# Kernel tuning notes

Hardware: AMD Instinct MI355X
Metric: run time of the kernel (lower is better)

The kernel has to match this reference:

```python
import jax, jax.numpy as jnp
import numpy as np

D_HEAD = 64
NEG_INF = jnp.float32(-jnp.inf)


def setup_inputs() -> dict:
    key = jax.random.key(0)
    ks = jax.random.split(key, 6)
    B, S, D, N, H = 8, 1024, 768, 12, 64
    init = 0.02
    return {
        "normalized_resid_pre": jax.random.normal(ks[0], (B, S, D), jnp.float32),
        "W_Q": jax.random.normal(ks[1], (N, D, H), jnp.float32) * init,
        "W_K": jax.random.normal(ks[2], (N, D, H), jnp.float32) * init,
        "W_V": jax.random.normal(ks[3], (N, D, H), jnp.float32) * init,
        "W_O": jax.random.normal(ks[4], (N, H, D), jnp.float32) * init,
        "b_Q": jnp.zeros((N, H), jnp.float32),
        "b_K": jnp.zeros((N, H), jnp.float32),
        "b_V": jnp.zeros((N, H), jnp.float32),
        "b_O": jnp.zeros((D,), jnp.float32),
    }


def _causal_mask(attn_scores):
    # Faithful to the source: keep entries where triu(scores, 1) != scores
    # (i.e. lower triangle incl. diagonal), set the rest to -inf.
    return jnp.where(jnp.triu(attn_scores, k=1) != attn_scores, attn_scores, NEG_INF)


def reference(normalized_resid_pre, W_Q, W_K, W_V, W_O, b_Q, b_K, b_V, b_O):
    x = normalized_resid_pre  # [b, p, d]
    keys = jnp.einsum('bpd,ndh->bpnh', x, W_K) + b_K
    queries = jnp.einsum('bpd,ndh->bpnh', x, W_Q) + b_Q
    attn_scores = jnp.einsum('bknh,bqnh->bnqk', keys, queries)  # [b, n, s_q, s_k]
    attn_probs = jax.nn.softmax(_causal_mask(attn_scores / np.sqrt(D_HEAD)), axis=-1)
    values = jnp.einsum('bpd,ndh->bpnh', x, W_V) + b_V
    z = jnp.einsum('bknh,bnqk->bqnh', values, attn_probs)
    attn_out = jnp.einsum('bpnh,nhe->bpe', z, W_O) + b_O
    return attn_out
```

## Files before the change

kernel.cpp:

```cpp
#include <hip/hip_runtime.h>
#include <stdint.h>

typedef __attribute__((ext_vector_type(4))) float f32x4;
typedef __attribute__((ext_vector_type(8))) __bf16 bf16v8;
typedef __attribute__((ext_vector_type(8))) unsigned short u16x8;
typedef __attribute__((ext_vector_type(4))) unsigned short u16x4;
typedef unsigned short u16;

#define AS1 __attribute__((address_space(1)))
#define AS3 __attribute__((address_space(3)))

__device__ __forceinline__ u16 f2b(float f) {
  union { __bf16 h; u16 u; } c; c.h = (__bf16)f; return c.u;
}

__device__ __forceinline__ f32x4 mfma16(bf16v8 a, bf16v8 b, f32x4 c) {
  return __builtin_amdgcn_mfma_f32_16x16x32_bf16(a, b, c, 0, 0, 0);
}

__device__ __forceinline__ void gl_lds16(const void* g, void* l) {
  __builtin_amdgcn_global_load_lds((AS1 void*)g, (AS3 void*)l, 16, 0, 0);
}

__global__ __launch_bounds__(256) void pack_x_kernel(
    const float* __restrict__ x, u16* __restrict__ xb, int n8,
    const float* __restrict__ bq, const float* __restrict__ bk,
    float* __restrict__ bc, float sq) {
  int i = blockIdx.x * 256 + threadIdx.x;
  if (i < n8) {
    const f32x4* p = (const f32x4*)(x + (size_t)i * 8);
    f32x4 a = p[0], b = p[1];
    u16x8 o;
    o[0] = f2b(a[0]); o[1] = f2b(a[1]); o[2] = f2b(a[2]); o[3] = f2b(a[3]);
    o[4] = f2b(b[0]); o[5] = f2b(b[1]); o[6] = f2b(b[2]); o[7] = f2b(b[3]);
    *(u16x8*)(xb + (size_t)i * 8) = o;
  } else {
    int j = i - n8;
    if (j < 768) bc[j] = bq[j] * sq;
    else if (j < 1536) bc[j] = bk[j - 768];
  }
}

__global__ __launch_bounds__(256) void pack_w_all(
    const float* __restrict__ wq, const float* __restrict__ wk,
    const float* __restrict__ wv, const float* __restrict__ wo,
    u16* __restrict__ btqk, u16* __restrict__ wvt, u16* __restrict__ wot,
    float sq) {
  __shared__ float t[64][65];
  const int z = blockIdx.z;
  const int which = z / 12, n = z % 12;
  const int c = threadIdx.x & 63, w = threadIdx.x >> 6;

  const float* in; u16* out; int in_rs, out_ns; float scale;
  int a0, b0;
  if (which == 0) { in = wq; out = btqk;          in_rs = 64;  out_ns = 49152; scale = sq;  }
  else if (which == 1) { in = wk; out = btqk + 589824; in_rs = 64; out_ns = 49152; scale = 1.f; }
  else if (which == 2) { in = wv; out = wvt;      in_rs = 64;  out_ns = 49152; scale = 1.f; }
  else { in = wo; out = wot;                      in_rs = 768; out_ns = 64;    scale = 1.f; }
  if (which < 3) { a0 = blockIdx.x * 64; b0 = 0; }
  else           { a0 = 0; b0 = blockIdx.x * 64; }

  const float* ip = in + (size_t)n * 49152;
#pragma unroll
  for (int i = 0; i < 16; ++i) {
    int r = i * 4 + w;
    t[r][c] = ip[(size_t)(a0 + r) * in_rs + (b0 + c)];
  }
  __syncthreads();
  u16* op = out + (size_t)n * out_ns;
#pragma unroll
  for (int i = 0; i < 16; ++i) {
    int r = i * 4 + w;
    op[(size_t)(b0 + r) * 768 + (a0 + c)] = f2b(t[c][r] * scale);
  }
}

template <int OUTF32, int BIASROW, int TN>
__global__ __launch_bounds__(256, 3) void gemm_bt(
    const u16* __restrict__ A, const u16* __restrict__ Bt,
    void* __restrict__ Cv, const float* __restrict__ bias, float scale, int N) {
  constexpr int K = 768;
  constexpr int MI = (TN == 128) ? 4 : 2;
  __shared__ u16 lA[2][128 * 32];
  __shared__ u16 lB[2][TN * 32];
  constexpr int BBUF = TN * 64;

  const int tid = threadIdx.x;
  const int lane = tid & 63, wid = tid >> 6;
  const int g = lane >> 4, l16 = lane & 15;
  const int rowb = (TN == 128) ? (wid >> 1) * 64 : wid * 32;
  const int colb = (TN == 128) ? (wid & 1) * 64 : 0;
  const int m0 = blockIdx.x * 128, n0 = blockIdx.y * TN;

  const int srow = tid >> 2;
  const int scol = (tid & 3) * 16;

  f32x4 acc[MI][4];
#pragma unroll
  for (int i = 0; i < MI; ++i)
#pragma unroll
    for (int j = 0; j < 4; ++j) acc[i][j] = (f32x4)0.f;

  const char* Ab = (const char*)(A + (size_t)m0 * K);
  const char* Bb = (const char*)(Bt + (size_t)n0 * K);
  char* lAb = (char*)&lA[0][0];
  char* lBb = (char*)&lB[0][0];

#define STAGE(buf, kt)                                                          \
  do {                                                                          \
    int kb = (kt) * 64;                                                         \
    gl_lds16(Ab + (size_t)srow * 1536 + kb + scol,                              \
             lAb + (buf) * 8192 + wid * 1024);                                  \
    gl_lds16(Ab + (size_t)(64 + srow) * 1536 + kb + scol,                       \
             lAb + (buf) * 8192 + 4096 + wid * 1024);                           \
    if (TN == 128) {                                                            \
      gl_lds16(Bb + (size_t)srow * 1536 + kb + scol,                            \
               lBb + (buf) * BBUF + wid * 1024);                                \
      gl_lds16(Bb + (size_t)(64 + srow) * 1536 + kb + scol,                     \
               lBb + (buf) * BBUF + 4096 + wid * 1024);                         \
    } else if (srow < 64) {                                                     \
      gl_lds16(Bb + (size_t)srow * 1536 + kb + scol,                            \
               lBb + (buf) * BBUF + wid * 1024);                                \
    }                                                                           \
  } while (0)

  STAGE(0, 0);
  __syncthreads();

  for (int kt = 0; kt < 24; ++kt) {
    const int cur = kt & 1;
    if (kt + 1 < 24) STAGE(cur ^ 1, kt + 1);
    bf16v8 af[MI], bfv[4];
#pragma unroll
    for (int i = 0; i < MI; ++i)
      af[i] = *(const bf16v8*)&lA[cur][(rowb + i * 16 + l16) * 32 + g * 8];
#pragma unroll
    for (int j = 0; j < 4; ++j)
      bfv[j] = *(const bf16v8*)&lB[cur][(colb + j * 16 + l16) * 32 + g * 8];
#pragma unroll
    for (int i = 0; i < MI; ++i)
#pragma unroll
      for (int j = 0; j < 4; ++j)
        acc[i][j] = mfma16(af[i], bfv[j], acc[i][j]);
    __syncthreads();
  }
#undef STAGE

  const int row0 = m0 + rowb, col0 = n0 + colb;
#pragma unroll
  for (int j = 0; j < 4; ++j) {
    const int col = col0 + j * 16 + l16;
    const float bcol = BIASROW ? 0.f : bias[col];
#pragma unroll
    for (int i = 0; i < MI; ++i) {
#pragma unroll
      for (int r = 0; r < 4; ++r) {
        const int row = row0 + i * 16 + g * 4 + r;
        const float bv = BIASROW ? bias[row] : bcol;
        const float v = (acc[i][j][r] + bv) * scale;
        if (OUTF32) ((float*)Cv)[(size_t)row * N + col] = v;
        else        ((u16*)Cv)[(size_t)row * N + col] = f2b(v);
      }
    }
  }
}

__global__ __launch_bounds__(256, 3) void flash7_kernel(
    const u16* __restrict__ QK, const u16* __restrict__ Vt,
    u16* __restrict__ Z) {
  __shared__ u16 lK[2][64 * 64];
  __shared__ u16 lV[2][64 * 64];
  __shared__ u16 lP[64 * 72];

  const int tid = threadIdx.x;
  const int lane = tid & 63, wid = tid >> 6;
  const int g = lane >> 4, l16 = lane & 15;

  const int id = blockIdx.x;
  const int xs = id & 7;
  const int rest = id >> 3;
  const int p = rest & 7;
  const int j = rest >> 3;
  const int head = xs + 8 * j;
  const int b = head / 12, n = head % 12;

  const int nchA = 16 - p;
  const int total = 17;

  const u16* Qh = QK + (size_t)b * 1024 * 1536 + n * 64;
  const u16* Kh = Qh + 768;
  const u16* Vh = Vt + (size_t)n * 64 * 8192 + b * 1024;
  u16* Zh = Z + (size_t)b * 1024 * 768 + n * 64;
  u16* myP = &lP[(wid * 16) * 72];

  const int srow8 = lane >> 3;
  const int sslot = lane & 7;
  const int scol = ((sslot ^ srow8) << 4);

#define FSTAGE(buf, c)                                                        \
  do {                                                                        \
    const int kv0_ = (c) << 6;                                                \
    const char* kb_ = (const char*)Kh + (size_t)(kv0_ + (wid << 4)) * 3072;   \
    const char* vb_ = (const char*)Vh + (size_t)(wid << 4) * 16384 +          \
                      (size_t)kv0_ * 2;                                       \
    gl_lds16(kb_ + (size_t)srow8 * 3072 + scol,                               \
             (char*)&lK[buf][0] + (wid << 11));                               \
    gl_lds16(kb_ + (size_t)(8 + srow8) * 3072 + scol,                         \
             (char*)&lK[buf][0] + (wid << 11) + 1024);                        \
    gl_lds16(vb_ + (size_t)srow8 * 16384 + scol,                              \
             (char*)&lV[buf][0] + (wid << 11));                               \
    gl_lds16(vb_ + (size_t)(8 + srow8) * 16384 + scol,                        \
             (char*)&lV[buf][0] + (wid << 11) + 1024);                        \
  } while (0)

#define SWZ(row, slot) (((row) << 6) + ((((slot) ^ ((row) & 7))) << 3))

  const int qwA = (15 - p) * 64 + wid * 16;
  const int qwB = p * 64 + wid * 16;
  bf16v8 qfA[2], qfB[2];
#pragma unroll
  for (int kk = 0; kk < 2; ++kk) {
    qfA[kk] = *(const bf16v8*)(Qh + (size_t)(qwA + l16) * 1536 + kk * 32 + g * 8);
    qfB[kk] = *(const bf16v8*)(Qh + (size_t)(qwB + l16) * 1536 + kk * 32 + g * 8);
  }

  f32x4 po[4];
#pragma unroll
  for (int ht = 0; ht < 4; ++ht) po[ht] = (f32x4)0.f;
  float m = -3e38f, l = 0.f;

  FSTAGE(0, 0);

  for (int s = 0; s < total; ++s) {
    const int cur = s & 1;
    const bool phB = s >= nchA;
    const int c = phB ? s - nchA : s;
    const int kv0 = c << 6;
    const int qw = phB ? qwB : qwA;

    if (s + 1 < total) {
      const int s1 = s + 1;
      const int c1 = (s1 >= nchA) ? s1 - nchA : s1;
      FSTAGE(cur ^ 1, c1);
      asm volatile("s_waitcnt vmcnt(4)" ::: "memory");
    } else {
      asm volatile("s_waitcnt vmcnt(0)" ::: "memory");
    }
    __builtin_amdgcn_s_barrier();
    __builtin_amdgcn_sched_barrier(0);

    const bf16v8 q0 = phB ? qfB[0] : qfA[0];
    const bf16v8 q1 = phB ? qfB[1] : qfA[1];

    bf16v8 kf[4][2];
#pragma unroll
    for (int kvt = 0; kvt < 4; ++kvt)
#pragma unroll
      for (int kk = 0; kk < 2; ++kk)
        kf[kvt][kk] =
            *(const bf16v8*)&lK[cur][SWZ(kvt * 16 + l16, kk * 4 + g)];
    f32x4 s_[4];
#pragma unroll
    for (int kvt = 0; kvt < 4; ++kvt) {
      f32x4 a = (f32x4)0.f;
      a = mfma16(kf[kvt][0], q0, a);
      a = mfma16(kf[kvt][1], q1, a);
      s_[kvt] = a;
    }
    bf16v8 vf[4][2];
#pragma unroll
    for (int ht = 0; ht < 4; ++ht)
#pragma unroll
      for (int kk = 0; kk < 2; ++kk)
        vf[ht][kk] =
            *(const bf16v8*)&lV[cur][SWZ(ht * 16 + l16, kk * 4 + g)];

    if (kv0 + 63 > qw) {
      const int qq = qw + l16;
#pragma unroll
      for (int kvt = 0; kvt < 4; ++kvt) {
        const int kv = kv0 + kvt * 16 + g * 4;
#pragma unroll
        for (int r = 0; r < 4; ++r)
          if (kv + r > qq) s_[kvt][r] = -3e38f;
      }
    }
    {
      float cm = s_[0][0];
#pragma unroll
      for (int kvt = 0; kvt < 4; ++kvt)
#pragma unroll
        for (int r = 0; r < 4; ++r) cm = fmaxf(cm, s_[kvt][r]);
      cm = fmaxf(cm, __shfl_xor(cm, 16));
      cm = fmaxf(cm, __shfl_xor(cm, 32));
      const bool defer = __all(cm - m <= 8.0f);
      float scl = 1.0f;
      if (!defer) {
        const float mn = fmaxf(m, cm);
        scl = exp2f(m - mn);
        m = mn;
#pragma unroll
        for (int r = 0; r < 4; ++r) {
          const float sr = __shfl(scl, g * 4 + r);
#pragma unroll
          for (int ht = 0; ht < 4; ++ht) po[ht][r] *= sr;
        }
      }
      float rs = 0.f;
#pragma unroll
      for (int kvt = 0; kvt < 4; ++kvt) {
        u16x4 pw;
#pragma unroll
        for (int r = 0; r < 4; ++r) {
          const float pv = exp2f(s_[kvt][r] - m);
          rs += pv;
          pw[r] = f2b(pv);
        }
        *(u16x4*)&myP[l16 * 72 + kvt * 16 + g * 4] = pw;
      }
      rs += __shfl_xor(rs, 16);
      rs += __shfl_xor(rs, 32);
      l = l * scl + rs;
    }
    bf16v8 pa[2];
#pragma unroll
    for (int kk = 0; kk < 2; ++kk)
      pa[kk] = *(const bf16v8*)&myP[l16 * 72 + kk * 32 + g * 8];
#pragma unroll
    for (int ht = 0; ht < 4; ++ht) {
      po[ht] = mfma16(pa[0], vf[ht][0], po[ht]);
      po[ht] = mfma16(pa[1], vf[ht][1], po[ht]);
    }

    __builtin_amdgcn_s_barrier();

    if (s == nchA - 1 || s == total - 1) {
#pragma unroll
      for (int r = 0; r < 4; ++r) {
        const float lr = __shfl(l, g * 4 + r);
        const float inv = 1.f / lr;
        const int qq = qw + g * 4 + r;
#pragma unroll
        for (int ht = 0; ht < 4; ++ht)
          Zh[(size_t)qq * 768 + ht * 16 + l16] = f2b(po[ht][r] * inv);
      }
      m = -3e38f;
      l = 0.f;
#pragma unroll
      for (int ht = 0; ht < 4; ++ht) po[ht] = (f32x4)0.f;
    }
  }
#undef FSTAGE
#undef SWZ
}

extern "C" void kernel_launch(void* const* d_in, const int* in_sizes, int n_in,
                              void* d_out, int out_size, void* d_ws,
                              size_t ws_size, hipStream_t stream) {
  const float* x  = (const float*)d_in[0];
  const float* wq = (const float*)d_in[1];
  const float* wk = (const float*)d_in[2];
  const float* wv = (const float*)d_in[3];
  const float* wo = (const float*)d_in[4];
  const float* bq = (const float*)d_in[5];
  const float* bk = (const float*)d_in[6];
  const float* bv = (const float*)d_in[7];
  const float* bo = (const float*)d_in[8];
  float* out = (float*)d_out;

  const float sq = 0.18033688011112042f;

  char* ws = (char*)d_ws;
  u16* Xb   = (u16*)ws; ws += 12582912;
  u16* BtQK = (u16*)ws; ws += 2359296;
  u16* WvT  = (u16*)ws; ws += 1179648;
  u16* WoT  = (u16*)ws; ws += 1179648;
  float* bc = (float*)ws; ws += 6144;
  u16* QKb  = (u16*)ws; ws += 25165824;
  u16* Vtb  = (u16*)ws; ws += 12582912;
  u16* Zb   = (u16*)ws; ws += 12582912;

  pack_x_kernel<<<3078, 256, 0, stream>>>(x, Xb, 786432, bq, bk, bc, sq);
  pack_w_all<<<dim3(12, 1, 48), 256, 0, stream>>>(wq, wk, wv, wo, BtQK, WvT,
                                                  WoT, sq);

  gemm_bt<0, 0, 128><<<dim3(64, 12), 256, 0, stream>>>(Xb, BtQK, QKb, bc,
                                                       1.0f, 1536);
  gemm_bt<0, 1, 64><<<dim3(6, 128), 256, 0, stream>>>(WvT, Xb, Vtb, bv, 1.0f,
                                                      8192);

  flash7_kernel<<<dim3(768), 256, 0, stream>>>(QKb, Vtb, Zb);

  gemm_bt<1, 0, 64><<<dim3(64, 12), 256, 0, stream>>>(Zb, WoT, out, bo, 1.0f,
                                                      768);
}
```

Baseline: 118.5 us.

## Fuse Q/K/V projections into a single GEMM with 192-wide tiles

```diff
diff --git a/kernel.cpp b/kernel.cpp
--- a/kernel.cpp
+++ b/kernel.cpp
@@ -25,7 +25,7 @@
 __global__ __launch_bounds__(256) void pack_x_kernel(
     const float* __restrict__ x, u16* __restrict__ xb, int n8,
     const float* __restrict__ bq, const float* __restrict__ bk,
-    float* __restrict__ bc, float sq) {
+    const float* __restrict__ bv, float* __restrict__ bc, float sq) {
   int i = blockIdx.x * 256 + threadIdx.x;
   if (i < n8) {
     const f32x4* p = (const f32x4*)(x + (size_t)i * 8);
@@ -38,25 +38,25 @@
     int j = i - n8;
     if (j < 768) bc[j] = bq[j] * sq;
     else if (j < 1536) bc[j] = bk[j - 768];
+    else if (j < 2304) bc[j] = bv[j - 1536];
   }
 }
 
 __global__ __launch_bounds__(256) void pack_w_all(
     const float* __restrict__ wq, const float* __restrict__ wk,
     const float* __restrict__ wv, const float* __restrict__ wo,
-    u16* __restrict__ btqk, u16* __restrict__ wvt, u16* __restrict__ wot,
-    float sq) {
+    u16* __restrict__ btqkv, u16* __restrict__ wot, float sq) {
   __shared__ float t[64][65];
   const int z = blockIdx.z;
   const int which = z / 12, n = z % 12;
   const int c = threadIdx.x & 63, w = threadIdx.x >> 6;
 
-  const float* in; u16* out; int in_rs, out_ns; float scale;
+  const float* in; u16* out; int in_rs; float scale;
   int a0, b0;
-  if (which == 0) { in = wq; out = btqk;          in_rs = 64;  out_ns = 49152; scale = sq;  }
-  else if (which == 1) { in = wk; out = btqk + 589824; in_rs = 64; out_ns = 49152; scale = 1.f; }
-  else if (which == 2) { in = wv; out = wvt;      in_rs = 64;  out_ns = 49152; scale = 1.f; }
-  else { in = wo; out = wot;                      in_rs = 768; out_ns = 64;    scale = 1.f; }
+  if (which == 0)      { in = wq; out = btqkv;           in_rs = 64;  scale = sq;  }
+  else if (which == 1) { in = wk; out = btqkv + 589824;  in_rs = 64;  scale = 1.f; }
+  else if (which == 2) { in = wv; out = btqkv + 1179648; in_rs = 64;  scale = 1.f; }
+  else                 { in = wo; out = wot;             in_rs = 768; scale = 1.f; }
   if (which < 3) { a0 = blockIdx.x * 64; b0 = 0; }
   else           { a0 = 0; b0 = blockIdx.x * 64; }
 
@@ -67,7 +67,7 @@
     t[r][c] = ip[(size_t)(a0 + r) * in_rs + (b0 + c)];
   }
   __syncthreads();
-  u16* op = out + (size_t)n * out_ns;
+  u16* op = out + (size_t)n * ((which < 3) ? 49152 : 64);
 #pragma unroll
   for (int i = 0; i < 16; ++i) {
     int r = i * 4 + w;
@@ -75,93 +75,173 @@
   }
 }
 
-template <int OUTF32, int BIASROW, int TN>
-__global__ __launch_bounds__(256, 3) void gemm_bt(
+__global__ __launch_bounds__(256, 3) void gemm_qkv(
     const u16* __restrict__ A, const u16* __restrict__ Bt,
-    void* __restrict__ Cv, const float* __restrict__ bias, float scale, int N) {
-  constexpr int K = 768;
-  constexpr int MI = (TN == 128) ? 4 : 2;
+    u16* __restrict__ QKb, u16* __restrict__ Vtb,
+    const float* __restrict__ bias) {
   __shared__ u16 lA[2][128 * 32];
-  __shared__ u16 lB[2][TN * 32];
-  constexpr int BBUF = TN * 64;
+  __shared__ u16 lB[2][192 * 32];
 
   const int tid = threadIdx.x;
   const int lane = tid & 63, wid = tid >> 6;
   const int g = lane >> 4, l16 = lane & 15;
-  const int rowb = (TN == 128) ? (wid >> 1) * 64 : wid * 32;
-  const int colb = (TN == 128) ? (wid & 1) * 64 : 0;
-  const int m0 = blockIdx.x * 128, n0 = blockIdx.y * TN;
+  const int wr = wid >> 1, wc = wid & 1;
+  const int m0 = blockIdx.x * 128, n0 = blockIdx.y * 192;
 
   const int srow = tid >> 2;
   const int scol = (tid & 3) * 16;
 
-  f32x4 acc[MI][4];
-#pragma unroll
-  for (int i = 0; i < MI; ++i)
-#pragma unroll
-    for (int j = 0; j < 4; ++j) acc[i][j] = (f32x4)0.f;
-
-  const char* Ab = (const char*)(A + (size_t)m0 * K);
-  const char* Bb = (const char*)(Bt + (size_t)n0 * K);
+  f32x4 acc[4][6];
+#pragma unroll
+  for (int i = 0; i < 4; ++i)
+#pragma unroll
+    for (int j = 0; j < 6; ++j) acc[i][j] = (f32x4)0.f;
+
+  const char* Ab = (const char*)(A + (size_t)m0 * 768);
+  const char* Bb = (const char*)(Bt + (size_t)n0 * 768);
   char* lAb = (char*)&lA[0][0];
   char* lBb = (char*)&lB[0][0];
 
-#define STAGE(buf, kt)                                                          \
+#define QSTAGE(buf, kt)                                                         \
   do {                                                                          \
     int kb = (kt) * 64;                                                         \
     gl_lds16(Ab + (size_t)srow * 1536 + kb + scol,                              \
              lAb + (buf) * 8192 + wid * 1024);                                  \
     gl_lds16(Ab + (size_t)(64 + srow) * 1536 + kb + scol,                       \
              lAb + (buf) * 8192 + 4096 + wid * 1024);                           \
-    if (TN == 128) {                                                            \
-      gl_lds16(Bb + (size_t)srow * 1536 + kb + scol,                            \
-               lBb + (buf) * BBUF + wid * 1024);                                \
-      gl_lds16(Bb + (size_t)(64 + srow) * 1536 + kb + scol,                     \
-               lBb + (buf) * BBUF + 4096 + wid * 1024);                         \
-    } else if (srow < 64) {                                                     \
-      gl_lds16(Bb + (size_t)srow * 1536 + kb + scol,                            \
-               lBb + (buf) * BBUF + wid * 1024);                                \
-    }                                                                           \
+    gl_lds16(Bb + (size_t)srow * 1536 + kb + scol,                              \
+             lBb + (buf) * 12288 + wid * 1024);                                 \
+    gl_lds16(Bb + (size_t)(64 + srow) * 1536 + kb + scol,                       \
+             lBb + (buf) * 12288 + 4096 + wid * 1024);                          \
+    gl_lds16(Bb + (size_t)(128 + srow) * 1536 + kb + scol,                      \
+             lBb + (buf) * 12288 + 8192 + wid * 1024);                          \
   } while (0)
 
-  STAGE(0, 0);
+  QSTAGE(0, 0);
   __syncthreads();
 
   for (int kt = 0; kt < 24; ++kt) {
     const int cur = kt & 1;
-    if (kt + 1 < 24) STAGE(cur ^ 1, kt + 1);
-    bf16v8 af[MI], bfv[4];
-#pragma unroll
-    for (int i = 0; i < MI; ++i)
+    if (kt + 1 < 24) QSTAGE(cur ^ 1, kt + 1);
+    bf16v8 af[4], bfv[6];
+#pragma unroll
+    for (int i = 0; i < 4; ++i)
+      af[i] = *(const bf16v8*)&lA[cur][(wr * 64 + i * 16 + l16) * 32 + g * 8];
+#pragma unroll
+    for (int j = 0; j < 6; ++j)
+      bfv[j] = *(const bf16v8*)&lB[cur][(wc * 96 + j * 16 + l16) * 32 + g * 8];
+#pragma unroll
+    for (int i = 0; i < 4; ++i)
+#pragma unroll
+      for (int j = 0; j < 6; ++j)
+        acc[i][j] = mfma16(af[i], bfv[j], acc[i][j]);
+    __syncthreads();
+  }
+#undef QSTAGE
+
+  const int row0 = m0 + wr * 64, col0 = n0 + wc * 96;
+  if (n0 < 1536) {
+#pragma unroll
+    for (int j = 0; j < 6; ++j) {
+      const int col = col0 + j * 16 + l16;
+      const float bcol = bias[col];
+#pragma unroll
+      for (int i = 0; i < 4; ++i)
+#pragma unroll
+        for (int r = 0; r < 4; ++r) {
+          const int row = row0 + i * 16 + g * 4 + r;
+          QKb[(size_t)row * 1536 + col] = f2b(acc[i][j][r] + bcol);
+        }
+    }
+  } else {
+#pragma unroll
+    for (int j = 0; j < 6; ++j) {
+      const int col = col0 + j * 16 + l16;
+      const float bcol = bias[col];
+      const size_t vrow = (size_t)(col - 1536) * 8192;
+#pragma unroll
+      for (int i = 0; i < 4; ++i) {
+        u16x4 pw;
+#pragma unroll
+        for (int r = 0; r < 4; ++r) pw[r] = f2b(acc[i][j][r] + bcol);
+        *(u16x4*)&Vtb[vrow + row0 + i * 16 + g * 4] = pw;
+      }
+    }
+  }
+}
+
+__global__ __launch_bounds__(256, 3) void gemm_o(
+    const u16* __restrict__ A, const u16* __restrict__ Bt,
+    float* __restrict__ C, const float* __restrict__ bias) {
+  __shared__ u16 lA[2][128 * 32];
+  __shared__ u16 lB[2][64 * 32];
+
+  const int tid = threadIdx.x;
+  const int lane = tid & 63, wid = tid >> 6;
+  const int g = lane >> 4, l16 = lane & 15;
+  const int rowb = wid * 32;
+  const int m0 = blockIdx.x * 128, n0 = blockIdx.y * 64;
+
+  const int srow = tid >> 2;
+  const int scol = (tid & 3) * 16;
+
+  f32x4 acc[2][4];
+#pragma unroll
+  for (int i = 0; i < 2; ++i)
+#pragma unroll
+    for (int j = 0; j < 4; ++j) acc[i][j] = (f32x4)0.f;
+
+  const char* Ab = (const char*)(A + (size_t)m0 * 768);
+  const char* Bb = (const char*)(Bt + (size_t)n0 * 768);
+  char* lAb = (char*)&lA[0][0];
+  char* lBb = (char*)&lB[0][0];
+
+#define OSTAGE(buf, kt)                                                         \
+  do {                                                                          \
+    int kb = (kt) * 64;                                                         \
+    gl_lds16(Ab + (size_t)srow * 1536 + kb + scol,                              \
+             lAb + (buf) * 8192 + wid * 1024);                                  \
+    gl_lds16(Ab + (size_t)(64 + srow) * 1536 + kb + scol,                       \
+             lAb + (buf) * 8192 + 4096 + wid * 1024);                           \
+    if (srow < 64)                                                              \
+      gl_lds16(Bb + (size_t)srow * 1536 + kb + scol,                            \
+               lBb + (buf) * 4096 + wid * 1024);                                \
+  } while (0)
+
+  OSTAGE(0, 0);
+  __syncthreads();
+
+  for (int kt = 0; kt < 24; ++kt) {
+    const int cur = kt & 1;
+    if (kt + 1 < 24) OSTAGE(cur ^ 1, kt + 1);
+    bf16v8 af[2], bfv[4];
+#pragma unroll
+    for (int i = 0; i < 2; ++i)
       af[i] = *(const bf16v8*)&lA[cur][(rowb + i * 16 + l16) * 32 + g * 8];
 #pragma unroll
     for (int j = 0; j < 4; ++j)
-      bfv[j] = *(const bf16v8*)&lB[cur][(colb + j * 16 + l16) * 32 + g * 8];
-#pragma unroll
-    for (int i = 0; i < MI; ++i)
+      bfv[j] = *(const bf16v8*)&lB[cur][(j * 16 + l16) * 32 + g * 8];
+#pragma unroll
+    for (int i = 0; i < 2; ++i)
 #pragma unroll
       for (int j = 0; j < 4; ++j)
         acc[i][j] = mfma16(af[i], bfv[j], acc[i][j]);
     __syncthreads();
   }
-#undef STAGE
-
-  const int row0 = m0 + rowb, col0 = n0 + colb;
+#undef OSTAGE
+
+  const int row0 = m0 + rowb;
 #pragma unroll
   for (int j = 0; j < 4; ++j) {
-    const int col = col0 + j * 16 + l16;
-    const float bcol = BIASROW ? 0.f : bias[col];
-#pragma unroll
-    for (int i = 0; i < MI; ++i) {
+    const int col = n0 + j * 16 + l16;
+    const float bcol = bias[col];
+#pragma unroll
+    for (int i = 0; i < 2; ++i)
 #pragma unroll
       for (int r = 0; r < 4; ++r) {
         const int row = row0 + i * 16 + g * 4 + r;
-        const float bv = BIASROW ? bias[row] : bcol;
-        const float v = (acc[i][j][r] + bv) * scale;
-        if (OUTF32) ((float*)Cv)[(size_t)row * N + col] = v;
-        else        ((u16*)Cv)[(size_t)row * N + col] = f2b(v);
-      }
-    }
+        C[(size_t)row * 768 + col] = acc[i][j][r] + bcol;
+      }
   }
 }
 
@@ -371,26 +451,21 @@
   const float sq = 0.18033688011112042f;
 
   char* ws = (char*)d_ws;
-  u16* Xb   = (u16*)ws; ws += 12582912;
-  u16* BtQK = (u16*)ws; ws += 2359296;
-  u16* WvT  = (u16*)ws; ws += 1179648;
-  u16* WoT  = (u16*)ws; ws += 1179648;
-  float* bc = (float*)ws; ws += 6144;
-  u16* QKb  = (u16*)ws; ws += 25165824;
-  u16* Vtb  = (u16*)ws; ws += 12582912;
-  u16* Zb   = (u16*)ws; ws += 12582912;
-
-  pack_x_kernel<<<3078, 256, 0, stream>>>(x, Xb, 786432, bq, bk, bc, sq);
-  pack_w_all<<<dim3(12, 1, 48), 256, 0, stream>>>(wq, wk, wv, wo, BtQK, WvT,
-                                                  WoT, sq);
-
-  gemm_bt<0, 0, 128><<<dim3(64, 12), 256, 0, stream>>>(Xb, BtQK, QKb, bc,
-                                                       1.0f, 1536);
-  gemm_bt<0, 1, 64><<<dim3(6, 128), 256, 0, stream>>>(WvT, Xb, Vtb, bv, 1.0f,
-                                                      8192);
+  u16* Xb    = (u16*)ws; ws += 12582912;
+  u16* BtQKV = (u16*)ws; ws += 3538944;
+  u16* WoT   = (u16*)ws; ws += 1179648;
+  float* bc  = (float*)ws; ws += 9216;
+  u16* QKb   = (u16*)ws; ws += 25165824;
+  u16* Vtb   = (u16*)ws; ws += 12582912;
+  u16* Zb    = (u16*)ws; ws += 12582912;
+
+  pack_x_kernel<<<3081, 256, 0, stream>>>(x, Xb, 786432, bq, bk, bv, bc, sq);
+  pack_w_all<<<dim3(12, 1, 48), 256, 0, stream>>>(wq, wk, wv, wo, BtQKV, WoT,
+                                                  sq);
+
+  gemm_qkv<<<dim3(64, 12), 256, 0, stream>>>(Xb, BtQKV, QKb, Vtb, bc);
 
   flash7_kernel<<<dim3(768), 256, 0, stream>>>(QKb, Vtb, Zb);
 
-  gemm_bt<1, 0, 64><<<dim3(64, 12), 256, 0, stream>>>(Zb, WoT, out, bo, 1.0f,
-                                                      768);
-}
+  gemm_o<<<dim3(64, 12), 256, 0, stream>>>(Zb, WoT, out, bo);
+}
```

Measured after the change: 106.6 us. -10.1%, faster.
